# Performance work log

Hardware: AMD Instinct MI355X
Metric: run time of the kernel (lower is better)

The kernel has to match this reference:

```python
import jax, jax.numpy as jnp
import numpy as np

NUM_CLASSES = 80
LAMBDA_OBJ, LAMBDA_NOOBJ, LAMBDA_BBOX, LAMBDA_CLASS = 1.0, 0.5, 5.0, 1.0
IOU_POS = 0.5
ALPHA, GAMMA = 0.25, 2.0


def setup_inputs() -> dict:
    key = jax.random.key(0)
    ks = jax.random.split(key, 7)
    B, A, H, W, C, M = 8, 3, 80, 80, NUM_CLASSES, 100
    objectness = jax.random.uniform(ks[0], (B, A, H, W, 1), dtype=jnp.float32)
    xy = jax.random.uniform(ks[1], (B, A, H, W, 2), dtype=jnp.float32)
    wh = 0.05 + 0.25 * jax.random.uniform(ks[2], (B, A, H, W, 2), dtype=jnp.float32)
    boxes = jnp.concatenate([xy, wh], axis=-1)  # (cx,cy,w,h)
    class_scores = jax.random.normal(ks[3], (B, A, H, W, C), dtype=jnp.float32)
    txy = jax.random.uniform(ks[4], (B, M, 2), dtype=jnp.float32)
    twh = 0.05 + 0.25 * jax.random.uniform(ks[5], (B, M, 2), dtype=jnp.float32)
    target_boxes = jnp.concatenate([txy, twh], axis=-1)
    target_labels = jax.random.randint(ks[6], (B, M), 0, C)
    return {"objectness": objectness, "boxes": boxes, "class_scores": class_scores,
            "target_boxes": target_boxes, "target_labels": target_labels}


def _box_iou(b1, b2):
    # b1: [N,4], b2: [M,4] in (cx,cy,w,h) -> IoU [N,M]
    b1_lo = b1[:, :2] - b1[:, 2:] * 0.5
    b1_hi = b1[:, :2] + b1[:, 2:] * 0.5
    b2_lo = b2[:, :2] - b2[:, 2:] * 0.5
    b2_hi = b2[:, :2] + b2[:, 2:] * 0.5
    lo = jnp.maximum(b1_lo[:, None, :], b2_lo[None, :, :])
    hi = jnp.minimum(b1_hi[:, None, :], b2_hi[None, :, :])
    wh = jnp.clip(hi - lo, 0.0)
    inter = wh[..., 0] * wh[..., 1]
    a1 = b1[:, 2] * b1[:, 3]
    a2 = b2[:, 2] * b2[:, 3]
    union = a1[:, None] + a2[None, :] - inter
    return inter / (union + 1e-6)


def _giou(b1, b2):
    # elementwise pairs [N,4],[N,4] -> [N]
    b1_lo = b1[:, :2] - b1[:, 2:] * 0.5
    b1_hi = b1[:, :2] + b1[:, 2:] * 0.5
    b2_lo = b2[:, :2] - b2[:, 2:] * 0.5
    b2_hi = b2[:, :2] + b2[:, 2:] * 0.5
    wh = jnp.clip(jnp.minimum(b1_hi, b2_hi) - jnp.maximum(b1_lo, b2_lo), 0.0)
    inter = wh[:, 0] * wh[:, 1]
    union = b1[:, 2] * b1[:, 3] + b2[:, 2] * b2[:, 3] - inter
    iou = inter / (union + 1e-6)
    ewh = jnp.clip(jnp.maximum(b1_hi, b2_hi) - jnp.minimum(b1_lo, b2_lo), 0.0)
    enclose = ewh[:, 0] * ewh[:, 1]
    return iou - (enclose - union) / (enclose + 1e-6)


def _per_image(obj, boxes, cls, tb, tl):
    # obj:[N], boxes:[N,4], cls:[N,C], tb:[M,4], tl:[M]
    N = boxes.shape[0]
    iou = _box_iou(boxes, tb)                 # [N,M] -- dominant intermediate
    max_iou = jnp.max(iou, axis=1)
    idx = jnp.argmax(iou, axis=1)
    pos = max_iou >= IOU_POS
    posf = pos.astype(boxes.dtype)
    bbox_t = tb[idx] * posf[:, None]          # zeros for negatives
    class_t = jnp.where(pos, tl[idx], 0)
    # objectness BCE (torch BCELoss clamps log terms at -100), summed over anchors
    logp = jnp.maximum(jnp.log(obj), -100.0)
    log1mp = jnp.maximum(jnp.log1p(-obj), -100.0)
    bce_sum = -jnp.sum(posf * logp + (1.0 - posf) * log1mp)
    pos_cnt = jnp.sum(posf)
    # faithful to source: scalar BCE sum broadcast over masks then re-summed
    obj_term = bce_sum * (LAMBDA_OBJ * pos_cnt + LAMBDA_NOOBJ * (N - pos_cnt))
    # GIoU bbox loss over positive anchors
    giou = _giou(boxes, bbox_t)
    bbox_sum = jnp.sum((1.0 - giou) * posf)
    # focal loss (logits) vs one-hot, mean over positive subset [P,C]
    onehot = jax.nn.one_hot(class_t, NUM_CLASSES, dtype=cls.dtype)
    p = jax.nn.sigmoid(cls)
    ce = jnp.maximum(cls, 0.0) - cls * onehot + jnp.log1p(jnp.exp(-jnp.abs(cls)))
    p_t = p * onehot + (1.0 - p) * (1.0 - onehot)
    a_t = ALPHA * onehot + (1.0 - ALPHA) * (1.0 - onehot)
    fl = a_t * (1.0 - p_t) ** GAMMA * ce
    class_sum = jnp.sum(fl * posf[:, None]) / jnp.maximum(pos_cnt * NUM_CLASSES, 1.0)
    return obj_term, bbox_sum, class_sum, pos_cnt


def _forward(objectness, boxes, class_scores, target_boxes, target_labels):
    B = objectness.shape[0]
    obj_f = objectness.reshape(B, -1)
    box_f = boxes.reshape(B, -1, 4)
    cls_f = class_scores.reshape(B, -1, NUM_CLASSES)
    o, bb, cl, pc = jax.vmap(_per_image)(obj_f, box_f, cls_f, target_boxes, target_labels)
    num_pos = jnp.maximum(jnp.sum(pc), 1.0)
    obj_loss = jnp.sum(o) / B
    bbox_loss = LAMBDA_BBOX * jnp.sum(bb) / num_pos
    class_loss = LAMBDA_CLASS * jnp.sum(cl) / B
    return obj_loss + bbox_loss + class_loss


def reference(objectness, boxes, class_scores, target_boxes, target_labels):
    return _forward(objectness, boxes, class_scores, target_boxes, target_labels)
```

## Files before the change

kernel.cpp:

```cpp
#include <hip/hip_runtime.h>
#include <math.h>

#define NCLS   80
#define MTGT   100
#define NANCH  19200
#define BATCH  8
#define NBLK   (NANCH / 256)

__device__ __forceinline__ float fast_rcp(float x) { return __builtin_amdgcn_rcpf(x); }

__device__ __forceinline__ float focal_term(float x, bool is_t) {
    const float ax  = fabsf(x);
    const float q   = __expf(-ax);
    const float ce0 = fmaxf(x, 0.0f) + __logf(1.0f + q);
    const float r   = fast_rcp(1.0f + q);
    const float p   = (x >= 0.0f) ? r : q * r;
    const float pt  = is_t ? (1.0f - p) : p;
    const float ce  = is_t ? (ce0 - x) : ce0;
    const float at  = is_t ? 0.25f : 0.75f;
    return at * pt * pt * ce;
}

__global__ __launch_bounds__(256) void anchor_kernel(
    const float* __restrict__ obj, const float* __restrict__ boxes,
    const float* __restrict__ cls, const float* __restrict__ tb,
    const int* __restrict__ tl, float4* __restrict__ partials)
{
    __shared__ float4 t_box[MTGT];
    __shared__ int    t_lab[MTGT];
    const int b   = blockIdx.y;
    const int tid = threadIdx.x;

    if (tid < MTGT) {
        const float4 t = ((const float4*)tb)[b * MTGT + tid];
        t_box[tid] = make_float4(t.x - 0.5f * t.z, t.y - 0.5f * t.w,
                                 t.x + 0.5f * t.z, t.y + 0.5f * t.w);
        t_lab[tid] = tl[b * MTGT + tid];
    }
    __syncthreads();

    const int i   = blockIdx.x * 256 + tid;
    const int gid = b * NANCH + i;

    const float4 bx = ((const float4*)boxes)[gid];
    const float lox = bx.x - 0.5f * bx.z, loy = bx.y - 0.5f * bx.w;
    const float hix = bx.x + 0.5f * bx.z, hiy = bx.y + 0.5f * bx.w;
    const float a1  = bx.z * bx.w;
    const float aa  = a1 + 1e-6f;

    float best = -1.0f; int bidx = 0;
    #pragma unroll 4
    for (int m = 0; m < MTGT; ++m) {
        const float4 t = t_box[m];
        float iw = fmaxf(fminf(hix, t.z) - fmaxf(lox, t.x), 0.0f);
        float ih = fmaxf(fminf(hiy, t.w) - fmaxf(loy, t.y), 0.0f);
        float inter = iw * ih;
        float area  = (t.z - t.x) * (t.w - t.y);
        float uni   = aa + area - inter;
        float iou   = inter * fast_rcp(uni);
        if (iou > best) { best = iou; bidx = m; }
    }

    const bool  pos  = (best >= 0.5f);
    const float posf = pos ? 1.0f : 0.0f;

    const float o   = obj[gid];
    const float bce = -fmaxf(__logf(pos ? o : 1.0f - o), -100.0f);

    float bbox_l = 0.0f;
    if (pos) {
        const float4 t = t_box[bidx];
        float iw = fmaxf(fminf(hix, t.z) - fmaxf(lox, t.x), 0.0f);
        float ih = fmaxf(fminf(hiy, t.w) - fmaxf(loy, t.y), 0.0f);
        float inter = iw * ih;
        float area  = (t.z - t.x) * (t.w - t.y);
        float uni   = a1 + area - inter;
        float iou   = inter * fast_rcp(uni + 1e-6f);
        float ew = fmaxf(fmaxf(hix, t.z) - fminf(lox, t.x), 0.0f);
        float eh = fmaxf(fmaxf(hiy, t.w) - fminf(loy, t.y), 0.0f);
        float enc  = ew * eh;
        float giou = iou - (enc - uni) * fast_rcp(enc + 1e-6f);
        bbox_l = 1.0f - giou;
    }

    const int lane = tid & 63;
    const int lab  = t_lab[bidx];
    float focal = 0.0f;
    unsigned long long pmask = __ballot(pos);
    while (pmask) {
        const int src = __ffsll((long long)pmask) - 1;
        pmask &= pmask - 1;
        const int g = __shfl(gid, src);
        const int c = __shfl(lab, src);
        const float* row = cls + (long)g * NCLS;
        focal += focal_term(row[lane], lane == c);
        if (lane < NCLS - 64) {
            const int j2 = lane + 64;
            focal += focal_term(row[j2], j2 == c);
        }
    }

    float v0 = bce, v1 = posf, v2 = bbox_l, v3 = focal;
    #pragma unroll
    for (int off = 32; off; off >>= 1) {
        v0 += __shfl_down(v0, off);
        v1 += __shfl_down(v1, off);
        v2 += __shfl_down(v2, off);
        v3 += __shfl_down(v3, off);
    }
    __shared__ float red[4][4];
    const int wave = tid >> 6;
    if (lane == 0) { red[wave][0] = v0; red[wave][1] = v1; red[wave][2] = v2; red[wave][3] = v3; }
    __syncthreads();
    if (tid == 0) {
        float s0 = 0.f, s1 = 0.f, s2 = 0.f, s3 = 0.f;
        #pragma unroll
        for (int w = 0; w < 4; ++w) {
            s0 += red[w][0]; s1 += red[w][1]; s2 += red[w][2]; s3 += red[w][3];
        }
        partials[b * NBLK + blockIdx.x] = make_float4(s0, s1, s2, s3);
    }
}

__global__ __launch_bounds__(512) void finalize_kernel(
    const float4* __restrict__ partials, float* __restrict__ out)
{
    const int wave = threadIdx.x >> 6;
    const int lane = threadIdx.x & 63;

    float s0 = 0.f, s1 = 0.f, s2 = 0.f, s3 = 0.f;
    for (int blk = lane; blk < NBLK; blk += 64) {
        const float4 p = partials[wave * NBLK + blk];
        s0 += p.x; s1 += p.y; s2 += p.z; s3 += p.w;
    }
    #pragma unroll
    for (int off = 32; off; off >>= 1) {
        s0 += __shfl_down(s0, off);
        s1 += __shfl_down(s1, off);
        s2 += __shfl_down(s2, off);
        s3 += __shfl_down(s3, off);
    }
    __shared__ float img[BATCH][4];
    if (lane == 0) { img[wave][0] = s0; img[wave][1] = s1; img[wave][2] = s2; img[wave][3] = s3; }
    __syncthreads();
    if (threadIdx.x == 0) {
        float sum_pc = 0.f, obj_l = 0.f, bbox_s = 0.f, cls_l = 0.f;
        #pragma unroll
        for (int b = 0; b < BATCH; ++b) {
            const float bce = img[b][0];
            const float pc  = img[b][1];
            const float bb  = img[b][2];
            const float fo  = img[b][3];
            sum_pc += pc;
            obj_l  += bce * (1.0f * pc + 0.5f * ((float)NANCH - pc));
            bbox_s += bb;
            cls_l  += fo / fmaxf(pc * (float)NCLS, 1.0f);
        }
        const float num_pos = fmaxf(sum_pc, 1.0f);
        out[0] = obj_l / (float)BATCH + 5.0f * bbox_s / num_pos + cls_l / (float)BATCH;
    }
}

extern "C" void kernel_launch(void* const* d_in, const int* in_sizes, int n_in,
                              void* d_out, int out_size, void* d_ws, size_t ws_size,
                              hipStream_t stream) {
    const float* obj   = (const float*)d_in[0];
    const float* boxes = (const float*)d_in[1];
    const float* cls   = (const float*)d_in[2];
    const float* tb    = (const float*)d_in[3];
    const int*   tl    = (const int*)d_in[4];
    float* out = (float*)d_out;

    float4* partials = (float4*)d_ws;

    dim3 gridA(NBLK, BATCH);
    anchor_kernel<<<gridA, 256, 0, stream>>>(obj, boxes, cls, tb, tl, partials);
    finalize_kernel<<<1, 512, 0, stream>>>(partials, out);
}
```

Measured before the change: 118.3 us.

## Use single-wave blocks, precompute target areas, drop cross-wave reduction

```diff
diff --git a/kernel.cpp b/kernel.cpp
--- a/kernel.cpp
+++ b/kernel.cpp
@@ -5,7 +5,8 @@
 #define MTGT   100
 #define NANCH  19200
 #define BATCH  8
-#define NBLK   (NANCH / 256)
+#define BLK    64
+#define NBLK   (NANCH / BLK)
 
 __device__ __forceinline__ float fast_rcp(float x) { return __builtin_amdgcn_rcpf(x); }
 
@@ -21,25 +22,27 @@
     return at * pt * pt * ce;
 }
 
-__global__ __launch_bounds__(256) void anchor_kernel(
+__global__ __launch_bounds__(BLK) void anchor_kernel(
     const float* __restrict__ obj, const float* __restrict__ boxes,
     const float* __restrict__ cls, const float* __restrict__ tb,
     const int* __restrict__ tl, float4* __restrict__ partials)
 {
     __shared__ float4 t_box[MTGT];
+    __shared__ float  t_area[MTGT];
     __shared__ int    t_lab[MTGT];
-    const int b   = blockIdx.y;
-    const int tid = threadIdx.x;
+    const int b    = blockIdx.y;
+    const int lane = threadIdx.x;
 
-    if (tid < MTGT) {
-        const float4 t = ((const float4*)tb)[b * MTGT + tid];
-        t_box[tid] = make_float4(t.x - 0.5f * t.z, t.y - 0.5f * t.w,
-                                 t.x + 0.5f * t.z, t.y + 0.5f * t.w);
-        t_lab[tid] = tl[b * MTGT + tid];
+    for (int m = lane; m < MTGT; m += BLK) {
+        const float4 t = ((const float4*)tb)[b * MTGT + m];
+        t_box[m]  = make_float4(t.x - 0.5f * t.z, t.y - 0.5f * t.w,
+                                t.x + 0.5f * t.z, t.y + 0.5f * t.w);
+        t_area[m] = t.z * t.w;
+        t_lab[m]  = tl[b * MTGT + m];
     }
     __syncthreads();
 
-    const int i   = blockIdx.x * 256 + tid;
+    const int i   = blockIdx.x * BLK + lane;
     const int gid = b * NANCH + i;
 
     const float4 bx = ((const float4*)boxes)[gid];
@@ -49,14 +52,13 @@
     const float aa  = a1 + 1e-6f;
 
     float best = -1.0f; int bidx = 0;
-    #pragma unroll 4
+    #pragma unroll 10
     for (int m = 0; m < MTGT; ++m) {
         const float4 t = t_box[m];
         float iw = fmaxf(fminf(hix, t.z) - fmaxf(lox, t.x), 0.0f);
         float ih = fmaxf(fminf(hiy, t.w) - fmaxf(loy, t.y), 0.0f);
         float inter = iw * ih;
-        float area  = (t.z - t.x) * (t.w - t.y);
-        float uni   = aa + area - inter;
+        float uni   = aa + t_area[m] - inter;
         float iou   = inter * fast_rcp(uni);
         if (iou > best) { best = iou; bidx = m; }
     }
@@ -73,8 +75,7 @@
         float iw = fmaxf(fminf(hix, t.z) - fmaxf(lox, t.x), 0.0f);
         float ih = fmaxf(fminf(hiy, t.w) - fmaxf(loy, t.y), 0.0f);
         float inter = iw * ih;
-        float area  = (t.z - t.x) * (t.w - t.y);
-        float uni   = a1 + area - inter;
+        float uni   = a1 + t_area[bidx] - inter;
         float iou   = inter * fast_rcp(uni + 1e-6f);
         float ew = fmaxf(fmaxf(hix, t.z) - fminf(lox, t.x), 0.0f);
         float eh = fmaxf(fmaxf(hiy, t.w) - fminf(loy, t.y), 0.0f);
@@ -83,8 +84,7 @@
         bbox_l = 1.0f - giou;
     }
 
-    const int lane = tid & 63;
-    const int lab  = t_lab[bidx];
+    const int lab = t_lab[bidx];
     float focal = 0.0f;
     unsigned long long pmask = __ballot(pos);
     while (pmask) {
@@ -108,18 +108,8 @@
         v2 += __shfl_down(v2, off);
         v3 += __shfl_down(v3, off);
     }
-    __shared__ float red[4][4];
-    const int wave = tid >> 6;
-    if (lane == 0) { red[wave][0] = v0; red[wave][1] = v1; red[wave][2] = v2; red[wave][3] = v3; }
-    __syncthreads();
-    if (tid == 0) {
-        float s0 = 0.f, s1 = 0.f, s2 = 0.f, s3 = 0.f;
-        #pragma unroll
-        for (int w = 0; w < 4; ++w) {
-            s0 += red[w][0]; s1 += red[w][1]; s2 += red[w][2]; s3 += red[w][3];
-        }
-        partials[b * NBLK + blockIdx.x] = make_float4(s0, s1, s2, s3);
-    }
+    if (lane == 0)
+        partials[b * NBLK + blockIdx.x] = make_float4(v0, v1, v2, v3);
 }
 
 __global__ __launch_bounds__(512) void finalize_kernel(
@@ -174,6 +164,6 @@
     float4* partials = (float4*)d_ws;
 
     dim3 gridA(NBLK, BATCH);
-    anchor_kernel<<<gridA, 256, 0, stream>>>(obj, boxes, cls, tb, tl, partials);
+    anchor_kernel<<<gridA, BLK, 0, stream>>>(obj, boxes, cls, tb, tl, partials);
     finalize_kernel<<<1, 512, 0, stream>>>(partials, out);
 }
```

After: 117.6 us. Within noise of the previous version (-0.6%).
